# Kernel optimization log

Hardware: AMD Instinct MI355X
Metric: run time of the kernel (lower is better)

## Reference

```python
import jax, jax.numpy as jnp
import numpy as np

B, CH_IN, D, H, W = 8, 256, 64, 16, 16
S = CH_IN // 2  # shurink = 128


def setup_inputs() -> dict:
    key = jax.random.key(0)
    ks = jax.random.split(key, 9)
    kstd = (2.0 / CH_IN) ** 0.5   # kaiming-like for 1x1 conv, fan_in = CH_IN
    ostd = (2.0 / S) ** 0.5
    x = jax.random.normal(ks[0], (B, CH_IN, D, H, W), dtype=jnp.float32)
    wk = jax.random.normal(ks[1], (S, CH_IN), dtype=jnp.float32) * kstd
    wq = jax.random.normal(ks[2], (S, CH_IN), dtype=jnp.float32) * kstd
    wv = jax.random.normal(ks[3], (S, CH_IN), dtype=jnp.float32) * kstd
    wo = jax.random.normal(ks[4], (CH_IN, S), dtype=jnp.float32) * ostd
    bk = jax.random.normal(ks[5], (S,), dtype=jnp.float32) * 0.01
    bq = jax.random.normal(ks[6], (S,), dtype=jnp.float32) * 0.01
    bv = jax.random.normal(ks[7], (S,), dtype=jnp.float32) * 0.01
    bo = jax.random.normal(ks[8], (CH_IN,), dtype=jnp.float32) * 0.01
    return {"x": x, "wk": wk, "bk": bk, "wq": wq, "bq": bq,
            "wv": wv, "bv": bv, "wo": wo, "bo": bo}


def reference(x, wk, bk, wq, bq, wv, bv, wo, bo):
    # 1x1x1 Conv3d == channel contraction: [B,C,D,H,W] x [S,C] -> [B,S,D,H,W]
    def proj(w, b):
        return jnp.einsum('bcdhw,oc->bodhw', x, w) + b[None, :, None, None, None]

    k = proj(wk, bk)  # [B,S,D,H,W]
    q = proj(wq, bq)
    v = proj(wv, bv)
    s_dim = k.shape[1]
    scale = 1.0 / jnp.sqrt(jnp.asarray(s_dim, x.dtype))
    # torch: bmm(k^T, q) over per-(b,h,w) [S,D] matrices -> [D_i, D_j]
    scores = jnp.einsum('bsihw,bsjhw->bhwij', k, q) * scale  # [B,H,W,D,D]
    # torch softmax(dim=1) on [BHW, D, D] == softmax over i (keys axis)
    a = jax.nn.softmax(scores, axis=3)
    # torch: bmm(v, a) -> [S, D_j]
    att = jnp.einsum('bsihw,bhwij->bsjhw', v, a)  # [B,S,D,H,W]
    out = jnp.einsum('bsdhw,cs->bcdhw', att, wo) + bo[None, :, None, None, None]
    return x + out  # atten_factor = 1
```

## Files before the change

kernel.cpp:

```cpp
#include <hip/hip_runtime.h>
#include <hip/hip_bf16.h>


typedef __bf16 bf16_t;
typedef bf16_t bf16x8 __attribute__((ext_vector_type(8)));
typedef bf16_t bf16x4 __attribute__((ext_vector_type(4)));
typedef float  f32x4  __attribute__((ext_vector_type(4)));

#define NB   8
#define NC   256
#define ND   64
#define NHW  256
#define NS   128

#define MFMA16 __builtin_amdgcn_mfma_f32_16x16x32_bf16

__device__ __forceinline__ int swz(int row, int col) {
  return col ^ ((row & 7) << 3);
}

__device__ __forceinline__ bf16x8 pack8(float4 a, float4 b) {
  bf16x8 r;
  r[0] = (bf16_t)a.x; r[1] = (bf16_t)a.y; r[2] = (bf16_t)a.z; r[3] = (bf16_t)a.w;
  r[4] = (bf16_t)b.x; r[5] = (bf16_t)b.y; r[6] = (bf16_t)b.z; r[7] = (bf16_t)b.w;
  return r;
}

__device__ __forceinline__ bf16x8 ldg_w8(const float* p) {
  float4 a = *(const float4*)p;
  float4 b = *(const float4*)(p + 4);
  return pack8(a, b);
}

__global__ __launch_bounds__(256) void transpose_x_w(
    const float* __restrict__ x,
    const float* __restrict__ wk, const float* __restrict__ wq,
    const float* __restrict__ wv, const float* __restrict__ wo,
    bf16_t* __restrict__ xT, bf16_t* __restrict__ wsW) {
  __shared__ bf16_t tile[64 * 72];
  const int bid = blockIdx.x;
  if (bid >= 8192) {
    const int wid = bid - 8192;
    const int mat = wid >> 3, sub = wid & 7;
    const int t = threadIdx.x;
    if (mat < 3) {
      const float* src = (mat == 0) ? wk : (mat == 1) ? wq : wv;
      bf16_t* dst = wsW + mat * 32768;
      int s = sub * 16 + (t >> 4), c0 = (t & 15) * 16;
      const float* p = src + s * NC + c0;
      float4 a0 = *(const float4*)p, a1 = *(const float4*)(p + 4);
      float4 a2 = *(const float4*)(p + 8), a3 = *(const float4*)(p + 12);
      *(bf16x8*)(dst + (c0 >> 3) * 1024 + s * 8)       = pack8(a0, a1);
      *(bf16x8*)(dst + ((c0 >> 3) + 1) * 1024 + s * 8) = pack8(a2, a3);
    } else {
      bf16_t* dst = wsW + 98304;
      int c = sub * 32 + (t >> 3), sc0 = (t & 7) * 16;
      const float* p = wo + c * NS + sc0;
      float4 a0 = *(const float4*)p, a1 = *(const float4*)(p + 4);
      float4 a2 = *(const float4*)(p + 8), a3 = *(const float4*)(p + 12);
      *(bf16x8*)(dst + (sc0 >> 3) * 2048 + c * 8)       = pack8(a0, a1);
      *(bf16x8*)(dst + ((sc0 >> 3) + 1) * 2048 + c * 8) = pack8(a2, a3);
    }
    return;
  }
  const int ct = bid & 3, hwt = (bid >> 2) & 3;
  const int d = (bid >> 4) & 63, b = bid >> 10;
  const int c0 = ct * 64, hw0 = hwt * 64;
  const int t = threadIdx.x;
  const int hwq = t & 15, chi = t >> 4;

  #pragma unroll
  for (int q = 0; q < 4; ++q) {
    int c = q * 16 + chi;
    float4 v4 = *(const float4*)(x + ((size_t)((b * NC + c0 + c) * ND + d)) * NHW + hw0 + hwq * 4);
    tile[(hwq * 4 + 0) * 72 + c] = (bf16_t)v4.x;
    tile[(hwq * 4 + 1) * 72 + c] = (bf16_t)v4.y;
    tile[(hwq * 4 + 2) * 72 + c] = (bf16_t)v4.z;
    tile[(hwq * 4 + 3) * 72 + c] = (bf16_t)v4.w;
  }
  __syncthreads();
  #pragma unroll
  for (int i = 0; i < 2; ++i) {
    int idx = t + 256 * i;
    int hw = idx >> 3, q = idx & 7;
    bf16x8 v8 = *(const bf16x8*)&tile[hw * 72 + q * 8];
    *(bf16x8*)(xT + ((size_t)((b * ND + d) * NHW + hw0 + hw)) * NC + c0 + q * 8) = v8;
  }
}

__global__ __launch_bounds__(256, 3) void qkv_attn3(
    const bf16_t* __restrict__ xT, const bf16_t* __restrict__ wsW,
    const float* __restrict__ bk, const float* __restrict__ bq,
    const float* __restrict__ bv, bf16_t* __restrict__ att) {
  __shared__ bf16_t lds[24576];
  bf16_t* kT   = lds;
  bf16_t* qT   = lds + 8192;
  bf16_t* vS   = lds + 16384;
  bf16_t* xTl  = lds;
  bf16_t* aT   = lds;
  bf16_t* attT = lds + 8192;

  const int gid = blockIdx.x;
  const int b = gid & 7, hw = gid >> 3;
  const int t = threadIdx.x, w = t >> 6, lane = t & 63;
  const int l16 = lane & 15, q4 = lane >> 4;

  const int mat = w >> 1;
  const int sb = (w & 1) * 64;
  const bf16_t* wm = mat ? (wsW + 32768) : wsW;
  const bf16_t* wvF = wsW + 65536;
  const float* bm = mat ? bq : bk;
  bf16_t* dstKQ = mat ? qT : kT;
  const int sbv = w * 32;

  f32x4 acc[4][4] = {};
  f32x4 accv[4][2] = {};

  for (int cc = 0; cc < 2; ++cc) {
    __syncthreads();
    #pragma unroll
    for (int jj = 0; jj < 4; ++jj) {
      int id = jj * 256 + t;
      int d = id >> 4, cg = (id & 15) * 8;
      bf16x8 v8 = *(const bf16x8*)(xT + ((size_t)((b * ND + d) * NHW + hw)) * NC + cc * 128 + cg);
      *(bf16x8*)&xTl[d * 128 + swz(d, cg)] = v8;
    }
    __syncthreads();
    #pragma unroll
    for (int ks = 0; ks < 4; ++ks) {
      const int kb = ks * 32 + q4 * 8;
      const int kgf = ((cc * 128 + kb) >> 3) * 1024;
      bf16x8 xfr[4], afk[4], bfv[2];
      #pragma unroll
      for (int i = 0; i < 4; ++i) {
        int row = i * 16 + l16;
        xfr[i] = *(const bf16x8*)&xTl[row * 128 + swz(row, kb)];
        int s = sb + i * 16 + l16;
        afk[i] = *(const bf16x8*)(wm + kgf + s * 8);
      }
      #pragma unroll
      for (int i = 0; i < 2; ++i) {
        int s = sbv + i * 16 + l16;
        bfv[i] = *(const bf16x8*)(wvF + kgf + s * 8);
      }
      #pragma unroll
      for (int nt = 0; nt < 4; ++nt)
        #pragma unroll
        for (int mt = 0; mt < 4; ++mt)
          acc[mt][nt] = MFMA16(afk[mt], xfr[nt], acc[mt][nt], 0, 0, 0);
      #pragma unroll
      for (int nt = 0; nt < 2; ++nt)
        #pragma unroll
        for (int mt = 0; mt < 4; ++mt)
          accv[mt][nt] = MFMA16(xfr[mt], bfv[nt], accv[mt][nt], 0, 0, 0);
    }
  }
  __syncthreads();

  #pragma unroll
  for (int mt = 0; mt < 4; ++mt) {
    int s0 = sb + mt * 16 + q4 * 4;
    float4 b4 = *(const float4*)(bm + s0);
    #pragma unroll
    for (int nt = 0; nt < 4; ++nt) {
      int d = nt * 16 + l16;
      bf16x4 pk;
      pk[0] = (bf16_t)(acc[mt][nt][0] + b4.x);
      pk[1] = (bf16_t)(acc[mt][nt][1] + b4.y);
      pk[2] = (bf16_t)(acc[mt][nt][2] + b4.z);
      pk[3] = (bf16_t)(acc[mt][nt][3] + b4.w);
      *(bf16x4*)&dstKQ[d * NS + swz(d, s0)] = pk;
    }
  }
  #pragma unroll
  for (int nt = 0; nt < 2; ++nt) {
    int s = sbv + nt * 16 + l16;
    float bvs = bv[s];
    #pragma unroll
    for (int mt = 0; mt < 4; ++mt) {
      int d0 = mt * 16 + q4 * 4;
      bf16x4 pv;
      pv[0] = (bf16_t)(accv[mt][nt][0] + bvs);
      pv[1] = (bf16_t)(accv[mt][nt][1] + bvs);
      pv[2] = (bf16_t)(accv[mt][nt][2] + bvs);
      pv[3] = (bf16_t)(accv[mt][nt][3] + bvs);
      *(bf16x4*)&vS[s * ND + (d0 ^ ((s & 7) << 3))] = pv;
    }
  }
  __syncthreads();

  float ps[16];
  {
    f32x4 sacc[4] = {};
    for (int ks = 0; ks < 4; ++ks) {
      const int kb = ks * 32 + q4 * 8;
      int jrow = w * 16 + l16;
      bf16x8 bfr = *(const bf16x8*)&qT[jrow * NS + swz(jrow, kb)];
      #pragma unroll
      for (int it = 0; it < 4; ++it) {
        int irow = it * 16 + l16;
        bf16x8 afr = *(const bf16x8*)&kT[irow * NS + swz(irow, kb)];
        sacc[it] = MFMA16(afr, bfr, sacc[it], 0, 0, 0);
      }
    }
    const float scale = 0.088388347648318447f;
    float mx = -1e30f;
    #pragma unroll
    for (int it = 0; it < 4; ++it)
      #pragma unroll
      for (int r = 0; r < 4; ++r) {
        float vv = sacc[it][r] * scale;
        ps[it * 4 + r] = vv;
        mx = fmaxf(mx, vv);
      }
    mx = fmaxf(mx, __shfl_xor(mx, 16));
    mx = fmaxf(mx, __shfl_xor(mx, 32));
    float sum = 0.f;
    #pragma unroll
    for (int i = 0; i < 16; ++i) { ps[i] = __expf(ps[i] - mx); sum += ps[i]; }
    sum += __shfl_xor(sum, 16);
    sum += __shfl_xor(sum, 32);
    float inv = 1.f / sum;
    #pragma unroll
    for (int i = 0; i < 16; ++i) ps[i] *= inv;
  }
  __syncthreads();

  {
    int j = w * 16 + l16;
    #pragma unroll
    for (int it = 0; it < 4; ++it) {
      bf16x4 pk;
      #pragma unroll
      for (int r = 0; r < 4; ++r) pk[r] = (bf16_t)ps[it * 4 + r];
      *(bf16x4*)&aT[j * ND + ((it * 16 + q4 * 4) ^ ((j & 7) << 3))] = pk;
    }
  }
  __syncthreads();

  {
    const int sbp = w * 32;
    f32x4 pacc[2][4] = {};
    #pragma unroll
    for (int ki = 0; ki < 2; ++ki) {
      const int kb = ki * 32 + q4 * 8;
      bf16x8 afr[2];
      #pragma unroll
      for (int mt = 0; mt < 2; ++mt) {
        int srow = sbp + mt * 16 + l16;
        afr[mt] = *(const bf16x8*)&vS[srow * ND + (kb ^ ((srow & 7) << 3))];
      }
      #pragma unroll
      for (int nt = 0; nt < 4; ++nt) {
        int jrow = nt * 16 + l16;
        bf16x8 bfr = *(const bf16x8*)&aT[jrow * ND + (kb ^ ((jrow & 7) << 3))];
        #pragma unroll
        for (int mt = 0; mt < 2; ++mt)
          pacc[mt][nt] = MFMA16(afr[mt], bfr, pacc[mt][nt], 0, 0, 0);
      }
    }
    #pragma unroll
    for (int nt = 0; nt < 4; ++nt) {
      int j = nt * 16 + l16;
      #pragma unroll
      for (int mt = 0; mt < 2; ++mt) {
        bf16x4 pk;
        #pragma unroll
        for (int r = 0; r < 4; ++r) pk[r] = (bf16_t)pacc[mt][nt][r];
        *(bf16x4*)&attT[j * NS + swz(j, sbp + mt * 16 + q4 * 4)] = pk;
      }
    }
  }
  __syncthreads();

  #pragma unroll
  for (int jj = 0; jj < 4; ++jj) {
    int f = jj * 2048 + t * 8;
    int d = f >> 7, s0 = f & 127;
    bf16x8 v8 = *(const bf16x8*)&attT[d * NS + (s0 ^ ((d & 7) << 3))];
    *(bf16x8*)(att + ((size_t)((b * ND + d) * NHW + hw)) * NS + s0) = v8;
  }
}

__global__ __launch_bounds__(256, 2) void out_proj(
    const bf16_t* __restrict__ att_ws,
    const bf16_t* __restrict__ woF, const float* __restrict__ bo,
    const float* __restrict__ x, float* __restrict__ out) {
  __shared__ union {
    bf16_t slab[256 * 128];
    float  stage[64 * 256];
  } sm;
  const int bid = blockIdx.x;
  const int ht = bid & 7, dc = (bid >> 3) & 7, ch = (bid >> 6) & 1, b = bid >> 7;
  const int t = threadIdx.x, w = t >> 6, lane = t & 63;
  const int l16 = lane & 15, g = lane >> 4;
  const int mh = w >> 1, nh = w & 1;

  {
    const int d = t >> 5, hw = t & 31;
    const bf16_t* src = att_ws + ((size_t)((b * ND + dc * 8 + d) * NHW + ht * 32 + hw)) * NS;
    const int row = d * 32 + hw;
    #pragma unroll
    for (int j = 0; j < 16; ++j) {
      bf16x8 v8 = *(const bf16x8*)(src + j * 8);
      *(bf16x8*)&sm.slab[row * NS + ((j ^ (hw & 7)) << 3)] = v8;
    }
  }
  __syncthreads();

  f32x4 acc[4][8] = {};
  #pragma unroll
  for (int kq = 0; kq < 4; ++kq) {
    bf16x8 af[4];
    #pragma unroll
    for (int mt = 0; mt < 4; ++mt) {
      int c = ch * 128 + mh * 64 + mt * 16 + l16;
      af[mt] = *(const bf16x8*)(woF + (kq * 4 + g) * 2048 + c * 8);
    }
    #pragma unroll
    for (int nt = 0; nt < 8; ++nt) {
      int dl = nh * 4 + (nt >> 1);
      int hwl = (nt & 1) * 16 + l16;
      int row = dl * 32 + hwl;
      bf16x8 bfr = *(const bf16x8*)&sm.slab[row * NS + (((kq * 4 + g) ^ (hwl & 7)) << 3)];
      #pragma unroll
      for (int mt = 0; mt < 4; ++mt)
        acc[mt][nt] = MFMA16(af[mt], bfr, acc[mt][nt], 0, 0, 0);
    }
  }

  #pragma unroll
  for (int p = 0; p < 2; ++p) {
    __syncthreads();
    if (mh == p) {
      #pragma unroll
      for (int mt = 0; mt < 4; ++mt) {
        #pragma unroll
        for (int nt = 0; nt < 8; ++nt) {
          int dl = nh * 4 + (nt >> 1);
          int hws = ((nt & 1) * 16 + l16) ^ (g << 3);
          int base = (mt * 16 + g * 4) * 256 + dl * 32 + hws;
          #pragma unroll
          for (int r = 0; r < 4; ++r)
            sm.stage[base + r * 256] = acc[mt][nt][r];
        }
      }
    }
    __syncthreads();
    #pragma unroll
    for (int ii = 0; ii < 16; ++ii) {
      int c6 = ii * 4 + w;
      int c = ch * 128 + p * 64 + c6;
      int dq = (lane >> 3) & 7;
      int hw4 = (lane & 7) * 4;
      float4 v = *(const float4*)&sm.stage[c6 * 256 + dq * 32 + (hw4 ^ ((ii & 3) << 3))];
      size_t gi = ((size_t)(b * NC + c) * ND + dc * 8 + dq) * NHW + ht * 32 + hw4;
      float4 xv = *(const float4*)(x + gi);
      float bias = bo[c];
      float4 o;
      o.x = v.x + bias + xv.x;
      o.y = v.y + bias + xv.y;
      o.z = v.z + bias + xv.z;
      o.w = v.w + bias + xv.w;
      *(float4*)(out + gi) = o;
    }
  }
}

struct SMemF {
  union {
    bf16_t xT[ND * NC];
    struct { bf16_t aT[ND * ND]; bf16_t attT[ND * NS]; } p2;
  } u;
  bf16_t kT[ND * NS];
  bf16_t qT[ND * NS];
  bf16_t vS[NS * ND];
};

__global__ __launch_bounds__(256) void attn_fused(
    const float* __restrict__ x,
    const float* __restrict__ wk, const float* __restrict__ bk,
    const float* __restrict__ wq, const float* __restrict__ bq,
    const float* __restrict__ wv, const float* __restrict__ bv,
    const float* __restrict__ wo, const float* __restrict__ bo,
    float* __restrict__ out) {
  __shared__ SMemF sm;
  const int gid = blockIdx.x;
  const int b = gid & 7;
  const int hw = gid >> 3;
  const int t = threadIdx.x;
  const int w = t >> 6;
  const int lane = t & 63;
  const int l16 = lane & 15;
  const int q4 = lane >> 4;
  const float* xb = x + (size_t)b * NC * ND * NHW + hw;
  {
    const int d = t & 63;
    const int cb = (t >> 6) * 64;
    for (int jj = 0; jj < 8; ++jj) {
      bf16x8 pk;
      #pragma unroll
      for (int e = 0; e < 8; ++e) {
        int c = cb + jj * 8 + e;
        pk[e] = (bf16_t)xb[(size_t)(c * ND + d) * NHW];
      }
      *(bf16x8*)&sm.u.xT[d * NC + swz(d, cb + jj * 8)] = pk;
    }
  }
  __syncthreads();
  {
    const int mat = w >> 1;
    const int sb = (w & 1) * 64;
    const float* wm = mat ? wq : wk;
    const float* bm = mat ? bq : bk;
    bf16_t* dst = mat ? sm.qT : sm.kT;
    f32x4 acc[4][4] = {};
    for (int ks = 0; ks < 8; ++ks) {
      const int kb = ks * 32 + q4 * 8;
      bf16x8 afr[4];
      #pragma unroll
      for (int mt = 0; mt < 4; ++mt) {
        int row = mt * 16 + l16;
        afr[mt] = *(const bf16x8*)&sm.u.xT[row * NC + swz(row, kb)];
      }
      #pragma unroll
      for (int st = 0; st < 4; ++st) {
        int s = sb + st * 16 + l16;
        bf16x8 bfr = ldg_w8(wm + s * NC + kb);
        #pragma unroll
        for (int mt = 0; mt < 4; ++mt)
          acc[mt][st] = MFMA16(afr[mt], bfr, acc[mt][st], 0, 0, 0);
      }
    }
    #pragma unroll
    for (int st = 0; st < 4; ++st) {
      int s = sb + st * 16 + l16;
      float bias = bm[s];
      #pragma unroll
      for (int mt = 0; mt < 4; ++mt) {
        #pragma unroll
        for (int r = 0; r < 4; ++r) {
          int d = mt * 16 + q4 * 4 + r;
          dst[d * NS + swz(d, s)] = (bf16_t)(acc[mt][st][r] + bias);
        }
      }
    }
  }
  {
    const int sb = w * 32;
    f32x4 acc[2][4] = {};
    for (int ks = 0; ks < 8; ++ks) {
      const int kb = ks * 32 + q4 * 8;
      bf16x8 afr[2];
      #pragma unroll
      for (int mt = 0; mt < 2; ++mt)
        afr[mt] = ldg_w8(wv + (sb + mt * 16 + l16) * NC + kb);
      #pragma unroll
      for (int nt = 0; nt < 4; ++nt) {
        int row = nt * 16 + l16;
        bf16x8 bfr = *(const bf16x8*)&sm.u.xT[row * NC + swz(row, kb)];
        #pragma unroll
        for (int mt = 0; mt < 2; ++mt)
          acc[mt][nt] = MFMA16(afr[mt], bfr, acc[mt][nt], 0, 0, 0);
      }
    }
    #pragma unroll
    for (int mt = 0; mt < 2; ++mt) {
      #pragma unroll
      for (int r = 0; r < 4; ++r) {
        int s = sb + mt * 16 + q4 * 4 + r;
        float bias = bv[s];
        #pragma unroll
        for (int nt = 0; nt < 4; ++nt) {
          int d = nt * 16 + l16;
          sm.vS[s * ND + swz(s, d)] = (bf16_t)(acc[mt][nt][r] + bias);
        }
      }
    }
  }
  __syncthreads();
  {
    f32x4 sacc[4] = {};
    for (int ks = 0; ks < 4; ++ks) {
      const int kb = ks * 32 + q4 * 8;
      int jrow = w * 16 + l16;
      bf16x8 bfr = *(const bf16x8*)&sm.qT[jrow * NS + swz(jrow, kb)];
      #pragma unroll
      for (int it = 0; it < 4; ++it) {
        int irow = it * 16 + l16;
        bf16x8 afr = *(const bf16x8*)&sm.kT[irow * NS + swz(irow, kb)];
        sacc[it] = MFMA16(afr, bfr, sacc[it], 0, 0, 0);
      }
    }
    const float scale = 0.088388347648318447f;
    float ps[16];
    float mx = -1e30f;
    #pragma unroll
    for (int it = 0; it < 4; ++it) {
      #pragma unroll
      for (int r = 0; r < 4; ++r) {
        float vv = sacc[it][r] * scale;
        ps[it * 4 + r] = vv;
        mx = fmaxf(mx, vv);
      }
    }
    mx = fmaxf(mx, __shfl_xor(mx, 16));
    mx = fmaxf(mx, __shfl_xor(mx, 32));
    float sum = 0.f;
    #pragma unroll
    for (int i = 0; i < 16; ++i) { ps[i] = __expf(ps[i] - mx); sum += ps[i]; }
    sum += __shfl_xor(sum, 16);
    sum += __shfl_xor(sum, 32);
    float inv = 1.f / sum;
    int j = w * 16 + l16;
    #pragma unroll
    for (int it = 0; it < 4; ++it) {
      bf16x4 pk;
      #pragma unroll
      for (int r = 0; r < 4; ++r) pk[r] = (bf16_t)(ps[it * 4 + r] * inv);
      *(bf16x4*)&sm.u.p2.aT[j * ND + swz(j, it * 16 + q4 * 4)] = pk;
    }
  }
  __syncthreads();
  {
    const int sb = w * 32;
    f32x4 acc[2][4] = {};
    #pragma unroll
    for (int ki = 0; ki < 2; ++ki) {
      const int kb = ki * 32 + q4 * 8;
      bf16x8 afr[2];
      #pragma unroll
      for (int mt = 0; mt < 2; ++mt) {
        int srow = sb + mt * 16 + l16;
        afr[mt] = *(const bf16x8*)&sm.vS[srow * ND + swz(srow, kb)];
      }
      #pragma unroll
      for (int nt = 0; nt < 4; ++nt) {
        int jrow = nt * 16 + l16;
        bf16x8 bfr = *(const bf16x8*)&sm.u.p2.aT[jrow * ND + swz(jrow, kb)];
        #pragma unroll
        for (int mt = 0; mt < 2; ++mt)
          acc[mt][nt] = MFMA16(afr[mt], bfr, acc[mt][nt], 0, 0, 0);
      }
    }
    #pragma unroll
    for (int nt = 0; nt < 4; ++nt) {
      int j = nt * 16 + l16;
      #pragma unroll
      for (int mt = 0; mt < 2; ++mt) {
        bf16x4 pk;
        #pragma unroll
        for (int r = 0; r < 4; ++r) pk[r] = (bf16_t)acc[mt][nt][r];
        *(bf16x4*)&sm.u.p2.attT[j * NS + swz(j, sb + mt * 16 + q4 * 4)] = pk;
      }
    }
  }
  __syncthreads();
  {
    const int cb = w * 64;
    f32x4 acc[4][4] = {};
    for (int ks = 0; ks < 4; ++ks) {
      const int kb = ks * 32 + q4 * 8;
      bf16x8 afr[4];
      #pragma unroll
      for (int mt = 0; mt < 4; ++mt)
        afr[mt] = ldg_w8(wo + (cb + mt * 16 + l16) * NS + kb);
      #pragma unroll
      for (int nt = 0; nt < 4; ++nt) {
        int jrow = nt * 16 + l16;
        bf16x8 bfr = *(const bf16x8*)&sm.u.p2.attT[jrow * NS + swz(jrow, kb)];
        #pragma unroll
        for (int mt = 0; mt < 4; ++mt)
          acc[mt][nt] = MFMA16(afr[mt], bfr, acc[mt][nt], 0, 0, 0);
      }
    }
    #pragma unroll
    for (int mt = 0; mt < 4; ++mt) {
      #pragma unroll
      for (int r = 0; r < 4; ++r) {
        int c = cb + mt * 16 + q4 * 4 + r;
        float bias = bo[c];
        #pragma unroll
        for (int nt = 0; nt < 4; ++nt) {
          int d = nt * 16 + l16;
          size_t gi = (size_t)(((b * NC + c) * ND + d) * NHW + hw);
          out[gi] = acc[mt][nt][r] + bias + x[gi];
        }
      }
    }
  }
}

extern "C" void kernel_launch(void* const* d_in, const int* in_sizes, int n_in,
                              void* d_out, int out_size, void* d_ws, size_t ws_size,
                              hipStream_t stream) {
  const float* x  = (const float*)d_in[0];
  const float* wk = (const float*)d_in[1];
  const float* bk = (const float*)d_in[2];
  const float* wq = (const float*)d_in[3];
  const float* bq = (const float*)d_in[4];
  const float* wv = (const float*)d_in[5];
  const float* bv = (const float*)d_in[6];
  const float* wo = (const float*)d_in[7];
  const float* bo = (const float*)d_in[8];
  float* out = (float*)d_out;

  const size_t need = (size_t)(131072 + 33554432 + 16777216) * 2;
  if (ws_size >= need) {
    bf16_t* wsW = (bf16_t*)d_ws;
    bf16_t* xT  = wsW + 131072;
    bf16_t* att = xT + 33554432;
    transpose_x_w<<<dim3(8224), dim3(256), 0, stream>>>(x, wk, wq, wv, wo, xT, wsW);
    qkv_attn3<<<dim3(2048), dim3(256), 0, stream>>>(xT, wsW, bk, bq, bv, att);
    out_proj<<<dim3(1024), dim3(256), 0, stream>>>(att, wsW + 98304, bo, x, out);
  } else {
    attn_fused<<<dim3(2048), dim3(256), 0, stream>>>(x, wk, bk, wq, bq, wv, bv, wo, bo, out);
  }
}
```

Before: 136.5 us.

## Swap MFMA operand roles in out_proj to store results directly without LDS staging

The output projection kernel now puts the attention slab (spatial positions) on the MFMA A operand and the weights on the B operand. Each lane's accumulator then holds four consecutive hw positions, so results plus bias and residual are written straight to global memory as float4, with no shared-memory staging pass or its extra barriers. The tile is halved to 128 rows, so the grid doubles to 2048 blocks and occupancy is raised to 4 blocks per SM with a smaller LDS footprint. The trade-off is that weight fragments are now reloaded from global memory by more blocks, and the global stores may be less coalesced, since 16 lanes write different channels.

```diff
diff --git a/kernel.cpp b/kernel.cpp
--- a/kernel.cpp
+++ b/kernel.cpp
@@ -282,86 +282,65 @@
   }
 }
 
-__global__ __launch_bounds__(256, 2) void out_proj(
+__global__ __launch_bounds__(256, 4) void out_proj2(
     const bf16_t* __restrict__ att_ws,
     const bf16_t* __restrict__ woF, const float* __restrict__ bo,
     const float* __restrict__ x, float* __restrict__ out) {
-  __shared__ union {
-    bf16_t slab[256 * 128];
-    float  stage[64 * 256];
-  } sm;
+  __shared__ bf16_t slab[128 * 128];
   const int bid = blockIdx.x;
-  const int ht = bid & 7, dc = (bid >> 3) & 7, ch = (bid >> 6) & 1, b = bid >> 7;
+  const int ht = bid & 7, dcq = (bid >> 3) & 15, ch = (bid >> 7) & 1, b = bid >> 8;
   const int t = threadIdx.x, w = t >> 6, lane = t & 63;
-  const int l16 = lane & 15, g = lane >> 4;
-  const int mh = w >> 1, nh = w & 1;
-
-  {
-    const int d = t >> 5, hw = t & 31;
-    const bf16_t* src = att_ws + ((size_t)((b * ND + dc * 8 + d) * NHW + ht * 32 + hw)) * NS;
-    const int row = d * 32 + hw;
-    #pragma unroll
-    for (int j = 0; j < 16; ++j) {
-      bf16x8 v8 = *(const bf16x8*)(src + j * 8);
-      *(bf16x8*)&sm.slab[row * NS + ((j ^ (hw & 7)) << 3)] = v8;
-    }
-  }
-  __syncthreads();
-
-  f32x4 acc[4][8] = {};
+  const int l16 = lane & 15, q4 = lane >> 4;
+
+  {
+    const int j = t & 15;
+    const int r0 = t >> 4;
+    #pragma unroll
+    for (int pp = 0; pp < 8; ++pp) {
+      int row = pp * 16 + r0;
+      int d = row >> 5, hw = row & 31;
+      bf16x8 v8 = *(const bf16x8*)(att_ws +
+          ((size_t)((b * ND + dcq * 4 + d) * NHW + ht * 32 + hw)) * NS + j * 8);
+      *(bf16x8*)&slab[row * NS + ((j ^ (hw & 7)) << 3)] = v8;
+    }
+  }
+  __syncthreads();
+
+  f32x4 acc[2][8] = {};
   #pragma unroll
   for (int kq = 0; kq < 4; ++kq) {
-    bf16x8 af[4];
-    #pragma unroll
-    for (int mt = 0; mt < 4; ++mt) {
-      int c = ch * 128 + mh * 64 + mt * 16 + l16;
-      af[mt] = *(const bf16x8*)(woF + (kq * 4 + g) * 2048 + c * 8);
+    bf16x8 af[2];
+    #pragma unroll
+    for (int mt = 0; mt < 2; ++mt) {
+      int row = (w * 2 + mt) * 16 + l16;
+      af[mt] = *(const bf16x8*)&slab[row * NS + (((kq * 4 + q4) ^ (row & 7)) << 3)];
     }
     #pragma unroll
     for (int nt = 0; nt < 8; ++nt) {
-      int dl = nh * 4 + (nt >> 1);
-      int hwl = (nt & 1) * 16 + l16;
-      int row = dl * 32 + hwl;
-      bf16x8 bfr = *(const bf16x8*)&sm.slab[row * NS + (((kq * 4 + g) ^ (hwl & 7)) << 3)];
-      #pragma unroll
-      for (int mt = 0; mt < 4; ++mt)
+      int c = ch * 128 + nt * 16 + l16;
+      bf16x8 bfr = *(const bf16x8*)(woF + (kq * 4 + q4) * 2048 + c * 8);
+      #pragma unroll
+      for (int mt = 0; mt < 2; ++mt)
         acc[mt][nt] = MFMA16(af[mt], bfr, acc[mt][nt], 0, 0, 0);
     }
   }
 
   #pragma unroll
-  for (int p = 0; p < 2; ++p) {
-    __syncthreads();
-    if (mh == p) {
-      #pragma unroll
-      for (int mt = 0; mt < 4; ++mt) {
-        #pragma unroll
-        for (int nt = 0; nt < 8; ++nt) {
-          int dl = nh * 4 + (nt >> 1);
-          int hws = ((nt & 1) * 16 + l16) ^ (g << 3);
-          int base = (mt * 16 + g * 4) * 256 + dl * 32 + hws;
-          #pragma unroll
-          for (int r = 0; r < 4; ++r)
-            sm.stage[base + r * 256] = acc[mt][nt][r];
-        }
-      }
-    }
-    __syncthreads();
-    #pragma unroll
-    for (int ii = 0; ii < 16; ++ii) {
-      int c6 = ii * 4 + w;
-      int c = ch * 128 + p * 64 + c6;
-      int dq = (lane >> 3) & 7;
-      int hw4 = (lane & 7) * 4;
-      float4 v = *(const float4*)&sm.stage[c6 * 256 + dq * 32 + (hw4 ^ ((ii & 3) << 3))];
-      size_t gi = ((size_t)(b * NC + c) * ND + dc * 8 + dq) * NHW + ht * 32 + hw4;
+  for (int mt = 0; mt < 2; ++mt) {
+    int mrow = w * 2 + mt;
+    int d = dcq * 4 + (mrow >> 1);
+    int hw0 = ht * 32 + (mrow & 1) * 16 + q4 * 4;
+    #pragma unroll
+    for (int nt = 0; nt < 8; ++nt) {
+      int c = ch * 128 + nt * 16 + l16;
+      size_t gi = ((size_t)(b * NC + c) * ND + d) * NHW + hw0;
       float4 xv = *(const float4*)(x + gi);
       float bias = bo[c];
       float4 o;
-      o.x = v.x + bias + xv.x;
-      o.y = v.y + bias + xv.y;
-      o.z = v.z + bias + xv.z;
-      o.w = v.w + bias + xv.w;
+      o.x = acc[mt][nt][0] + bias + xv.x;
+      o.y = acc[mt][nt][1] + bias + xv.y;
+      o.z = acc[mt][nt][2] + bias + xv.z;
+      o.w = acc[mt][nt][3] + bias + xv.w;
       *(float4*)(out + gi) = o;
     }
   }
@@ -612,7 +591,7 @@
     bf16_t* att = xT + 33554432;
     transpose_x_w<<<dim3(8224), dim3(256), 0, stream>>>(x, wk, wq, wv, wo, xT, wsW);
     qkv_attn3<<<dim3(2048), dim3(256), 0, stream>>>(xT, wsW, bk, bq, bv, att);
-    out_proj<<<dim3(1024), dim3(256), 0, stream>>>(att, wsW + 98304, bo, x, out);
+    out_proj2<<<dim3(2048), dim3(256), 0, stream>>>(att, wsW + 98304, bo, x, out);
   } else {
     attn_fused<<<dim3(2048), dim3(256), 0, stream>>>(x, wk, bk, wq, bq, wv, bv, wo, bo, out);
   }
```

Result: slower. 174.2 us (+27.7%).
